# Kernel tuning notes

Hardware: AMD Instinct MI355X
Metric: run time of the kernel (lower is better)

Reference implementation:

```python
import jax, jax.numpy as jnp
import numpy as np

N, E = 30000, 180000
IN, H, OUT = 3000, 512, 30


def _segment_softmax(e, dst, n):
    # numerically stable softmax over incoming edges of each destination node
    m = jax.ops.segment_max(e, dst, num_segments=n)
    m = jnp.where(jnp.isfinite(m), m, 0.0)  # nodes with no in-edges
    ex = jnp.exp(e - m[dst])
    den = jax.ops.segment_sum(ex, dst, num_segments=n)
    return ex / den[dst]


def _gat(x, src, dst, Ws, Wd, a_s, a_d, n, alpha=None):
    """edGATConv (heads=1, no self-loops, no bias).
    xs = lin_s(x); attention score from lin_s(x)[src] and lin_d(x)[dst];
    out[i] = sum_{e: dst_e=i} alpha_e * xs[src_e].
    If alpha is given (tie_alpha), reuse it instead of recomputing."""
    xs = x @ Ws.T  # [n, F_out]
    if alpha is None:
        xd = x @ Wd.T
        e = jax.nn.leaky_relu(xs[src] @ a_s + xd[dst] @ a_d, 0.2)  # [E]
        alpha = _segment_softmax(e, dst, n)
    out = jax.ops.segment_sum(alpha[:, None] * xs[src], dst, num_segments=n)
    return out, alpha


def setup_inputs() -> dict:
    key = jax.random.key(0)
    ks = jax.random.split(key, 7)
    features = jax.random.normal(ks[0], (N, IN), dtype=jnp.float32)
    edge_index = jax.random.randint(ks[1], (2, E), 0, N)
    W1s = jax.random.normal(ks[2], (H, IN), dtype=jnp.float32) * 0.02
    W1d = jax.random.normal(ks[3], (H, IN), dtype=jnp.float32) * 0.02
    a1s = jax.random.normal(ks[4], (H,), dtype=jnp.float32) * 0.1
    a1d = jax.random.normal(ks[5], (H,), dtype=jnp.float32) * 0.1
    W2s = jax.random.normal(ks[6], (OUT, H), dtype=jnp.float32) * 0.05
    return {"features": features, "edge_index": edge_index,
            "W1s": W1s, "W1d": W1d, "a1s": a1s, "a1d": a1d, "W2s": W2s}


def reference(features, edge_index, W1s, W1d, a1s, a1d, W2s):
    src, dst = edge_index[0], edge_index[1]
    n = features.shape[0]
    # conv1: attentive GAT layer, stores tie_alpha
    h1, alpha1 = _gat(features, src, dst, W1s, W1d, a1s, a1d, n)
    h1 = jax.nn.elu(h1)
    # conv2: aslinear=True -> plain linear with lin_s
    h2 = h1 @ W2s.T  # [N, OUT]
    # conv3: weights tied to conv2 transposed, alpha tied to conv1
    # W3s = W2s.T so xs3 = h2 @ W3s.T = h2 @ W2s
    h3, _ = _gat(h2, src, dst, W2s.T, None, None, None, n, alpha=alpha1)
    h3 = jax.nn.elu(h3)
    # conv4: aslinear, weight tied to conv1 transposed: h3 @ W4s.T = h3 @ W1s
    h4 = h3 @ W1s  # [N, IN]
    return (h2, h4)
```

## Files before the change

kernel.cpp:

```cpp
#include <hip/hip_runtime.h>

typedef unsigned short u16;
typedef __bf16 bf16_t;
typedef bf16_t bf16x8 __attribute__((ext_vector_type(8)));
typedef float f32x4 __attribute__((ext_vector_type(4)));
typedef u16 u16x8 __attribute__((ext_vector_type(8)));

#define AS1 __attribute__((address_space(1)))
#define AS3 __attribute__((address_space(3)))

__device__ __forceinline__ u16 f2bf(float f) {
    union { float f; unsigned u; } v; v.f = f;
    unsigned r = v.u + 0x7FFFu + ((v.u >> 16) & 1u);
    return (u16)(r >> 16);
}
__device__ __forceinline__ float bf2f(u16 s) {
    union { unsigned u; float f; } v; v.u = ((unsigned)s) << 16;
    return v.f;
}

__device__ __forceinline__ void gload_lds16(const u16* g, u16* l) {
    __builtin_amdgcn_global_load_lds((AS1 const void*)g, (AS3 void*)l, 16, 0, 0);
}

template <bool OUT_BF16, bool GUARD>
__global__ __launch_bounds__(256) void gemm_bt(
    const u16* __restrict__ A, const u16* __restrict__ B, void* __restrict__ Cv,
    int K, int ldc, int Mreal, int Nreal)
{
    __shared__ u16 As[128 * 64];
    __shared__ u16 Bs[128 * 64];
    const int t = threadIdx.x;
    const int w = t >> 6, l = t & 63;

    const int nwg = gridDim.x * gridDim.y;
    const int lin = blockIdx.y * gridDim.x + blockIdx.x;
    const int xcd = lin & 7, loc = lin >> 3;
    const int q = nwg >> 3, r = nwg & 7;
    const int swz = (xcd < r ? xcd * (q + 1) : r * (q + 1) + (xcd - r) * q) + loc;
    const int bx = swz % gridDim.x, by = swz / gridDim.x;

    const int m0 = by * 128, n0 = bx * 128;
    const int wm = (w >> 1) * 64, wn = (w & 1) * 64;

    const int srow = w << 5;
    const int lrow = l >> 3, lc = l & 7;

    f32x4 acc[4][4] = {};

    for (int kt = 0; kt < K; kt += 64) {
#pragma unroll
        for (int i = 0; i < 4; ++i) {
            int row = srow + i * 8 + lrow;
            int gc = ((lc ^ (row & 7)) << 3);
            const u16* ga = A + (size_t)(m0 + row) * K + kt + gc;
            const u16* gb = B + (size_t)(n0 + row) * K + kt + gc;
            u16* la = &As[(srow + i * 8) * 64];
            u16* lb = &Bs[(srow + i * 8) * 64];
            gload_lds16(ga, la);
            gload_lds16(gb, lb);
        }
        asm volatile("s_waitcnt vmcnt(0)");
        __syncthreads();

#pragma unroll
        for (int kk = 0; kk < 2; ++kk) {
            bf16x8 af[4], bfr[4];
            int kc = kk * 4 + (l >> 4);
#pragma unroll
            for (int mi = 0; mi < 4; ++mi) {
                int row = wm + mi * 16 + (l & 15);
                af[mi] = *(const bf16x8*)&As[row * 64 + ((kc ^ (row & 7)) << 3)];
            }
#pragma unroll
            for (int ni = 0; ni < 4; ++ni) {
                int col = wn + ni * 16 + (l & 15);
                bfr[ni] = *(const bf16x8*)&Bs[col * 64 + ((kc ^ (col & 7)) << 3)];
            }
#pragma unroll
            for (int mi = 0; mi < 4; ++mi)
#pragma unroll
                for (int ni = 0; ni < 4; ++ni)
                    acc[mi][ni] = __builtin_amdgcn_mfma_f32_16x16x32_bf16(
                        af[mi], bfr[ni], acc[mi][ni], 0, 0, 0);
        }
        __syncthreads();
    }

#pragma unroll
    for (int mi = 0; mi < 4; ++mi) {
#pragma unroll
        for (int qq = 0; qq < 4; ++qq) {
            int row = m0 + wm + mi * 16 + (l >> 4) * 4 + qq;
            if (GUARD && row >= Mreal) continue;
#pragma unroll
            for (int ni = 0; ni < 4; ++ni) {
                int col = n0 + wn + ni * 16 + (l & 15);
                if (GUARD && col >= Nreal) continue;
                float v = acc[mi][ni][qq];
                if (OUT_BF16) ((u16*)Cv)[(size_t)row * ldc + col] = f2bf(v);
                else          ((float*)Cv)[(size_t)row * ldc + col] = v;
            }
        }
    }
}

__global__ void k_prep(const float* __restrict__ W1d, const float* __restrict__ a1d,
                       const float* __restrict__ W1s, const float* __restrict__ a1s,
                       const float* __restrict__ W2s, const int* __restrict__ dst,
                       float* __restrict__ vd, float* __restrict__ vs,
                       u16* __restrict__ w1sb, u16* __restrict__ w1st,
                       u16* __restrict__ w2sb, unsigned* __restrict__ deg) {
    int b = blockIdx.x, t = threadIdx.x;
    if (b < 12) {
        int i = b * 256 + t;
        if (i >= 3000) return;
        float ad = 0.f, as = 0.f;
        for (int h = 0; h < 512; ++h) {
            ad += W1d[(size_t)h * 3000 + i] * a1d[h];
            as += W1s[(size_t)h * 3000 + i] * a1s[h];
        }
        vd[i] = ad;
        vs[i] = as;
    } else if (b < 1516) {
        int idx = (b - 12) * 256 + t;
        int n = idx / 752, k = (idx % 752) * 4;
        ushort4 o = make_ushort4(0, 0, 0, 0);
        if (k < 3000) {
            float4 v = *(const float4*)(W1s + (size_t)n * 3000 + k);
            o.x = f2bf(v.x); o.y = f2bf(v.y); o.z = f2bf(v.z); o.w = f2bf(v.w);
        }
        *(ushort4*)(w1sb + (size_t)n * 3008 + k) = o;
    } else if (b < 1900) {
        __shared__ float tile[64][65];
        int fb = b - 1516;
        int i0 = (fb % 48) * 64, h0 = (fb / 48) * 64;
        int il = t & 63, hq = t >> 6;
#pragma unroll
        for (int rr = 0; rr < 16; ++rr) {
            int hl = rr * 4 + hq;
            int i = i0 + il;
            tile[hl][il] = (i < 3000) ? W1s[(size_t)(h0 + hl) * 3000 + i] : 0.f;
        }
        __syncthreads();
#pragma unroll
        for (int rr = 0; rr < 16; ++rr) {
            int il2 = rr * 4 + hq;
            w1st[(size_t)(i0 + il2) * 512 + h0 + il] = f2bf(tile[il][il2]);
        }
    } else if (b < 2156) {
        int idx = (b - 1900) * 256 + t;
        int n = idx >> 9, k = idx & 511;
        w2sb[idx] = (n < 30) ? f2bf(W2s[(size_t)n * 512 + k]) : (u16)0;
    } else {
        int j = (b - 2156) * 256 + t;
        if (j < 180000) atomicAdd(&deg[dst[j]], 1u);
    }
}

__global__ void k_convX(const float* __restrict__ X, u16* __restrict__ xb,
                        const float* __restrict__ vd, const float* __restrict__ vs,
                        float* __restrict__ sd, float* __restrict__ ss) {
    __shared__ float redd[4], reds[4];
    int n = blockIdx.x, t = threadIdx.x;
    u16* brow = xb + (size_t)n * 3008;
    if (n < 30000) {
        const float* xrow = X + (size_t)n * 3000;
        float pd = 0.f, ps = 0.f;
#pragma unroll
        for (int it = 0; it < 3; ++it) {
            int c = (t + it * 256) * 4;
            if (c < 3000) {
                float4 v = *(const float4*)(xrow + c);
                float4 wd = *(const float4*)(vd + c);
                float4 wvs = *(const float4*)(vs + c);
                ushort4 o;
                o.x = f2bf(v.x); o.y = f2bf(v.y); o.z = f2bf(v.z); o.w = f2bf(v.w);
                pd += v.x * wd.x + v.y * wd.y + v.z * wd.z + v.w * wd.w;
                ps += v.x * wvs.x + v.y * wvs.y + v.z * wvs.z + v.w * wvs.w;
                *(ushort4*)(brow + c) = o;
            } else if (c < 3008) {
                *(ushort4*)(brow + c) = make_ushort4(0, 0, 0, 0);
            }
        }
#pragma unroll
        for (int s = 32; s; s >>= 1) {
            pd += __shfl_xor(pd, s);
            ps += __shfl_xor(ps, s);
        }
        if ((t & 63) == 0) { redd[t >> 6] = pd; reds[t >> 6] = ps; }
        __syncthreads();
        if (t == 0) {
            sd[n] = redd[0] + redd[1] + redd[2] + redd[3];
            ss[n] = reds[0] + reds[1] + reds[2] + reds[3];
        }
    } else {
#pragma unroll
        for (int it = 0; it < 3; ++it) {
            int c = (t + it * 256) * 4;
            if (c < 3008) *(ushort4*)(brow + c) = make_ushort4(0, 0, 0, 0);
        }
    }
}

__global__ void k_scan1(const unsigned* __restrict__ deg, unsigned* __restrict__ bsum, int n) {
    __shared__ unsigned ws[4];
    int i = blockIdx.x * 256 + threadIdx.x;
    unsigned v = (i < n) ? deg[i] : 0u;
#pragma unroll
    for (int s = 32; s; s >>= 1) v += __shfl_xor(v, s);
    if ((threadIdx.x & 63) == 0) ws[threadIdx.x >> 6] = v;
    __syncthreads();
    if (threadIdx.x == 0) bsum[blockIdx.x] = ws[0] + ws[1] + ws[2] + ws[3];
}

__global__ void k_scanB(const unsigned* __restrict__ deg, const unsigned* __restrict__ bsum,
                        unsigned* __restrict__ off, unsigned* __restrict__ cur,
                        int n, int nb) {
    __shared__ unsigned tmp[256];
    __shared__ unsigned bo;
    int b = blockIdx.x, t = threadIdx.x, i = b * 256 + t;
    if (t < 64) {
        unsigned s0 = (t < nb) ? bsum[t] : 0u;
        unsigned s1 = (t + 64 < nb) ? bsum[t + 64] : 0u;
        unsigned v = ((t < b) ? s0 : 0u) + ((t + 64 < b) ? s1 : 0u);
#pragma unroll
        for (int s = 32; s; s >>= 1) v += __shfl_xor(v, s);
        if (t == 0) bo = v;
        if (b == nb - 1) {
            unsigned tv = s0 + s1;
#pragma unroll
            for (int s = 32; s; s >>= 1) tv += __shfl_xor(tv, s);
            if (t == 0) off[n] = tv;
        }
    }
    __syncthreads();
    unsigned v = (i < n) ? deg[i] : 0u;
    tmp[t] = v;
    __syncthreads();
    for (int s = 1; s < 256; s <<= 1) {
        unsigned a = (t >= s) ? tmp[t - s] : 0u;
        __syncthreads();
        tmp[t] += a;
        __syncthreads();
    }
    if (i < n) {
        unsigned o = bo + tmp[t] - v;
        off[i] = o;
        cur[i] = o;
    }
}

__global__ void k_fill(const int* __restrict__ dst, unsigned* __restrict__ cur,
                       unsigned* __restrict__ csr) {
    int j = blockIdx.x * 256 + threadIdx.x;
    if (j >= 180000) return;
    unsigned pos = atomicAdd(&cur[dst[j]], 1u);
    csr[pos] = (unsigned)j;
}

__global__ void k_soft(const int* __restrict__ src, const float* __restrict__ ss,
                       const float* __restrict__ sd, float* __restrict__ alpha,
                       const unsigned* __restrict__ csr, const unsigned* __restrict__ off) {
    int t = threadIdx.x;
    int g = t >> 3, l = t & 7;
    int n = blockIdx.x * 32 + g;
    if (n >= 30000) return;
    unsigned lo = off[n], hi = off[n + 1];
    if (lo == hi) return;
    float sdn = sd[n];
    float m = -1e30f;
    for (unsigned i = lo + l; i < hi; i += 8) {
        float v = ss[src[csr[i]]] + sdn;
        v = v > 0.f ? v : 0.2f * v;
        m = fmaxf(m, v);
    }
    m = fmaxf(m, __shfl_xor(m, 1));
    m = fmaxf(m, __shfl_xor(m, 2));
    m = fmaxf(m, __shfl_xor(m, 4));
    float den = 0.f;
    for (unsigned i = lo + l; i < hi; i += 8) {
        float v = ss[src[csr[i]]] + sdn;
        v = v > 0.f ? v : 0.2f * v;
        den += expf(v - m);
    }
    den += __shfl_xor(den, 1);
    den += __shfl_xor(den, 2);
    den += __shfl_xor(den, 4);
    float inv = 1.f / den;
    for (unsigned i = lo + l; i < hi; i += 8) {
        unsigned j = csr[i];
        float v = ss[src[j]] + sdn;
        v = v > 0.f ? v : 0.2f * v;
        alpha[j] = expf(v - m) * inv;
    }
}

__global__ void k_agg(const u16* __restrict__ xin, const float* __restrict__ alpha,
                      const unsigned* __restrict__ csr, const unsigned* __restrict__ off,
                      const int* __restrict__ src, u16* __restrict__ outb, int nvalid) {
    int w = threadIdx.x >> 6, l = threadIdx.x & 63;
    int n = blockIdx.x * 4 + w;
    float acc[8] = {};
    if (n < nvalid) {
        unsigned lo = off[n], hi = off[n + 1];
        unsigned i = lo;
        for (; i + 2 <= hi; i += 2) {
            unsigned j0 = csr[i], j1 = csr[i + 1];
            float a0 = alpha[j0], a1 = alpha[j1];
            int s0 = src[j0], s1 = src[j1];
            u16x8 r0 = *(const u16x8*)&xin[(size_t)s0 * 512 + l * 8];
            u16x8 r1 = *(const u16x8*)&xin[(size_t)s1 * 512 + l * 8];
#pragma unroll
            for (int k = 0; k < 8; ++k) acc[k] += a0 * bf2f(r0[k]) + a1 * bf2f(r1[k]);
        }
        if (i < hi) {
            unsigned j0 = csr[i];
            float a0 = alpha[j0];
            int s0 = src[j0];
            u16x8 r0 = *(const u16x8*)&xin[(size_t)s0 * 512 + l * 8];
#pragma unroll
            for (int k = 0; k < 8; ++k) acc[k] += a0 * bf2f(r0[k]);
        }
    }
    u16x8 o;
#pragma unroll
    for (int k = 0; k < 8; ++k) {
        float a = acc[k] > 0.f ? acc[k] : expf(acc[k]) - 1.f;
        o[k] = f2bf(a);
    }
    *(u16x8*)&outb[(size_t)n * 512 + l * 8] = o;
}

__global__ void k_xs3(const float* __restrict__ h2, const float* __restrict__ W2s,
                      u16* __restrict__ xs3) {
    int t = threadIdx.x;
    size_t n0 = (size_t)blockIdx.x * 8;
    float w0[30], w1[30];
#pragma unroll
    for (int o = 0; o < 30; ++o) {
        w0[o] = W2s[(size_t)o * 512 + t];
        w1[o] = W2s[(size_t)o * 512 + t + 256];
    }
    for (int r = 0; r < 8; ++r) {
        size_t n = n0 + r;
        const float* hr = h2 + n * 30;
        float a0 = 0.f, a1 = 0.f;
#pragma unroll
        for (int o = 0; o < 30; ++o) {
            float v = hr[o];
            a0 += v * w0[o];
            a1 += v * w1[o];
        }
        xs3[n * 512 + t] = f2bf(a0);
        xs3[n * 512 + t + 256] = f2bf(a1);
    }
}

extern "C" void kernel_launch(void* const* d_in, const int* in_sizes, int n_in,
                              void* d_out, int out_size, void* d_ws, size_t ws_size,
                              hipStream_t stream) {
    const float* X   = (const float*)d_in[0];
    const int*   ei  = (const int*)d_in[1];
    const float* W1s = (const float*)d_in[2];
    const float* W1d = (const float*)d_in[3];
    const float* a1s = (const float*)d_in[4];
    const float* a1d = (const float*)d_in[5];
    const float* W2s = (const float*)d_in[6];
    const int* src = ei;
    const int* dst = ei + 180000;

    float* out = (float*)d_out;
    float* h2 = out;
    float* h4 = out + 900000;

    char* ob = (char*)(out + 900000);
    u16* xbf  = (u16*)ob;
    u16* xs1b = (u16*)(ob + 180961280);
    u16* h1b  = (u16*)(ob + 180961280 + 30801920);
    u16* xs3b = (u16*)(ob + 180961280 + 30801920 + 30801920);

    char* w = (char*)d_ws;
    auto carve = [&](size_t bytes) { char* p = w; w += (bytes + 255) & ~(size_t)255; return p; };
    u16* w1sb  = (u16*)carve((size_t)512 * 3008 * 2);
    u16* w1st  = (u16*)carve((size_t)3072 * 512 * 2);
    u16* w2sb  = (u16*)carve((size_t)128 * 512 * 2);
    u16* h3b   = (u16*)carve((size_t)30080 * 512 * 2);
    float* vd    = (float*)carve(3008 * 4);
    float* vs    = (float*)carve(3008 * 4);
    float* ss    = (float*)carve(30000 * 4);
    float* sd    = (float*)carve(30000 * 4);
    float* alpha = (float*)carve(180000 * 4);
    unsigned* deg = (unsigned*)carve(30000 * 4);
    unsigned* off = (unsigned*)carve(30004 * 4);
    unsigned* cur = (unsigned*)carve(30000 * 4);
    unsigned* csr = (unsigned*)carve(180000 * 4);
    unsigned* bsum = (unsigned*)carve(128 * 4);

    hipMemsetAsync(deg, 0, 30000 * 4, stream);

    k_prep<<<2860, 256, 0, stream>>>(W1d, a1d, W1s, a1s, W2s, dst,
                                     vd, vs, w1sb, w1st, w2sb, deg);

    k_convX<<<30080, 256, 0, stream>>>(X, xbf, vd, vs, sd, ss);

    gemm_bt<true, false><<<dim3(4, 235), 256, 0, stream>>>(xbf, w1sb, xs1b, 3008, 512, 0, 0);

    k_scan1<<<118, 256, 0, stream>>>(deg, bsum, 30000);
    k_scanB<<<118, 256, 0, stream>>>(deg, bsum, off, cur, 30000, 118);
    k_fill<<<704, 256, 0, stream>>>(dst, cur, csr);
    k_soft<<<938, 256, 0, stream>>>(src, ss, sd, alpha, csr, off);

    k_agg <<<7520, 256, 0, stream>>>(xs1b, alpha, csr, off, src, h1b, 30000);

    gemm_bt<false, true><<<dim3(1, 235), 256, 0, stream>>>(h1b, w2sb, h2, 512, 30, 30000, 30);

    k_xs3 <<<3750, 256, 0, stream>>>(h2, W2s, xs3b);
    k_agg <<<7520, 256, 0, stream>>>(xs3b, alpha, csr, off, src, h3b, 30000);

    gemm_bt<false, true><<<dim3(24, 235), 256, 0, stream>>>(h3b, w1st, h4, 512, 3000, 30000, 3000);
}
```

Before: 681.5 us.

## Fuse X bf16 conversion into first GEMM and aggregate layer-3 before projection

The first GEMM now reads fp32 features directly, converts them to bf16 into LDS and computes the attention score dot products in the bx==0 blocks. This removes the separate conversion kernel and its write and re-read of a bf16 copy of X. Layer 3 is reordered to aggregate the 30-wide h2 over edges first and then project to 512 with ELU. This uses linearity to shrink the gather width from 512 bf16 to 30 fp32. The trade-off is redundant fp32 A-loads across the four column blocks, which read X four times.

Measured after the change: 645.5 us. -5.3%, faster.

```diff
diff --git a/kernel.cpp b/kernel.cpp
--- a/kernel.cpp
+++ b/kernel.cpp
@@ -103,6 +103,148 @@
             }
         }
     }
+}
+
+__global__ __launch_bounds__(256) void gemm_xw2(
+    const float* __restrict__ X, const u16* __restrict__ Bw, u16* __restrict__ C,
+    const float* __restrict__ vd, const float* __restrict__ vs,
+    float* __restrict__ sd, float* __restrict__ ss)
+{
+    __shared__ u16 As[128 * 64];
+    __shared__ u16 Bs[2][128 * 64];
+    const int t = threadIdx.x;
+    const int w = t >> 6, l = t & 63;
+
+    const int nwg = gridDim.x * gridDim.y;
+    const int lin = blockIdx.y * gridDim.x + blockIdx.x;
+    const int xcd = lin & 7, loc = lin >> 3;
+    const int q = nwg >> 3, r = nwg & 7;
+    const int swz = (xcd < r ? xcd * (q + 1) : r * (q + 1) + (xcd - r) * q) + loc;
+    const int bx = swz % gridDim.x, by = swz / gridDim.x;
+
+    const int m0 = by * 128, n0 = bx * 128;
+    const int wm = (w >> 1) * 64, wn = (w & 1) * 64;
+    const int srow = w << 5;
+    const int lrow = l >> 3, lc = l & 7;
+
+    f32x4 acc[4][4] = {};
+    float sdp[4] = {}, ssp[4] = {};
+    const bool do_s = (bx == 0);
+
+    int rowg[4];
+    bool okr[4];
+#pragma unroll
+    for (int i = 0; i < 4; ++i) {
+        rowg[i] = m0 + srow + i * 8 + lrow;
+        okr[i] = rowg[i] < 30000;
+    }
+
+    float4 pa[4][2];
+    auto loadA = [&](int kt) {
+        int c = kt + lc * 8;
+        bool okc = c < 3000;
+#pragma unroll
+        for (int i = 0; i < 4; ++i) {
+            bool ok = okr[i] && okc;
+            const float* p = X + (ok ? ((size_t)rowg[i] * 3000 + c) : 0);
+            float4 v0 = *(const float4*)p;
+            float4 v1 = *(const float4*)(p + 4);
+            if (!ok) { v0 = make_float4(0.f, 0.f, 0.f, 0.f); v1 = v0; }
+            pa[i][0] = v0;
+            pa[i][1] = v1;
+        }
+    };
+    auto stageB = [&](int kt2, int buf) {
+#pragma unroll
+        for (int i = 0; i < 4; ++i) {
+            int row = srow + i * 8 + lrow;
+            int gc = ((lc ^ (row & 7)) << 3);
+            gload_lds16(Bw + (size_t)(n0 + row) * 3008 + kt2 + gc,
+                        &Bs[buf][(srow + i * 8) * 64]);
+        }
+    };
+
+    loadA(0);
+    stageB(0, 0);
+    int cur = 0;
+
+    for (int kt = 0; kt < 3008; kt += 64) {
+        if (do_s) {
+            int c = kt + lc * 8;
+            float4 d0 = *(const float4*)(vd + c);
+            float4 d1 = *(const float4*)(vd + c + 4);
+            float4 s0 = *(const float4*)(vs + c);
+            float4 s1 = *(const float4*)(vs + c + 4);
+#pragma unroll
+            for (int i = 0; i < 4; ++i) {
+                sdp[i] += pa[i][0].x * d0.x + pa[i][0].y * d0.y + pa[i][0].z * d0.z + pa[i][0].w * d0.w
+                        + pa[i][1].x * d1.x + pa[i][1].y * d1.y + pa[i][1].z * d1.z + pa[i][1].w * d1.w;
+                ssp[i] += pa[i][0].x * s0.x + pa[i][0].y * s0.y + pa[i][0].z * s0.z + pa[i][0].w * s0.w
+                        + pa[i][1].x * s1.x + pa[i][1].y * s1.y + pa[i][1].z * s1.z + pa[i][1].w * s1.w;
+            }
+        }
+#pragma unroll
+        for (int i = 0; i < 4; ++i) {
+            int row = srow + i * 8 + lrow;
+            u16x8 o;
+            o[0] = f2bf(pa[i][0].x); o[1] = f2bf(pa[i][0].y);
+            o[2] = f2bf(pa[i][0].z); o[3] = f2bf(pa[i][0].w);
+            o[4] = f2bf(pa[i][1].x); o[5] = f2bf(pa[i][1].y);
+            o[6] = f2bf(pa[i][1].z); o[7] = f2bf(pa[i][1].w);
+            *(u16x8*)&As[row * 64 + ((lc ^ (row & 7)) << 3)] = o;
+        }
+        loadA(kt + 64);
+        int ktn = (kt + 64 < 3008) ? kt + 64 : 2944;
+        stageB(ktn, cur ^ 1);
+        asm volatile("s_waitcnt vmcnt(12) lgkmcnt(0)" ::: "memory");
+        __builtin_amdgcn_s_barrier();
+
+#pragma unroll
+        for (int kk = 0; kk < 2; ++kk) {
+            bf16x8 af[4], bfr[4];
+            int kc = kk * 4 + (l >> 4);
+#pragma unroll
+            for (int mi = 0; mi < 4; ++mi) {
+                int row = wm + mi * 16 + (l & 15);
+                af[mi] = *(const bf16x8*)&As[row * 64 + ((kc ^ (row & 7)) << 3)];
+            }
+#pragma unroll
+            for (int ni = 0; ni < 4; ++ni) {
+                int col = wn + ni * 16 + (l & 15);
+                bfr[ni] = *(const bf16x8*)&Bs[cur][col * 64 + ((kc ^ (col & 7)) << 3)];
+            }
+#pragma unroll
+            for (int mi = 0; mi < 4; ++mi)
+#pragma unroll
+                for (int ni = 0; ni < 4; ++ni)
+                    acc[mi][ni] = __builtin_amdgcn_mfma_f32_16x16x32_bf16(
+                        af[mi], bfr[ni], acc[mi][ni], 0, 0, 0);
+        }
+        asm volatile("s_barrier" ::: "memory");
+        cur ^= 1;
+    }
+
+    if (do_s) {
+#pragma unroll
+        for (int i = 0; i < 4; ++i) {
+            float a = sdp[i], b = ssp[i];
+            a += __shfl_xor(a, 1); a += __shfl_xor(a, 2); a += __shfl_xor(a, 4);
+            b += __shfl_xor(b, 1); b += __shfl_xor(b, 2); b += __shfl_xor(b, 4);
+            if (lc == 0 && okr[i]) { sd[rowg[i]] = a; ss[rowg[i]] = b; }
+        }
+    }
+
+#pragma unroll
+    for (int mi = 0; mi < 4; ++mi)
+#pragma unroll
+        for (int qq = 0; qq < 4; ++qq) {
+            int row = m0 + wm + mi * 16 + (l >> 4) * 4 + qq;
+#pragma unroll
+            for (int ni = 0; ni < 4; ++ni) {
+                int col = n0 + wn + ni * 16 + (l & 15);
+                C[(size_t)row * 512 + col] = f2bf(acc[mi][qq == 0 ? ni : ni][qq]);
+            }
+        }
 }
 
 __global__ void k_prep(const float* __restrict__ W1d, const float* __restrict__ a1d,
@@ -155,51 +297,6 @@
     } else {
         int j = (b - 2156) * 256 + t;
         if (j < 180000) atomicAdd(&deg[dst[j]], 1u);
-    }
-}
-
-__global__ void k_convX(const float* __restrict__ X, u16* __restrict__ xb,
-                        const float* __restrict__ vd, const float* __restrict__ vs,
-                        float* __restrict__ sd, float* __restrict__ ss) {
-    __shared__ float redd[4], reds[4];
-    int n = blockIdx.x, t = threadIdx.x;
-    u16* brow = xb + (size_t)n * 3008;
-    if (n < 30000) {
-        const float* xrow = X + (size_t)n * 3000;
-        float pd = 0.f, ps = 0.f;
-#pragma unroll
-        for (int it = 0; it < 3; ++it) {
-            int c = (t + it * 256) * 4;
-            if (c < 3000) {
-                float4 v = *(const float4*)(xrow + c);
-                float4 wd = *(const float4*)(vd + c);
-                float4 wvs = *(const float4*)(vs + c);
-                ushort4 o;
-                o.x = f2bf(v.x); o.y = f2bf(v.y); o.z = f2bf(v.z); o.w = f2bf(v.w);
-                pd += v.x * wd.x + v.y * wd.y + v.z * wd.z + v.w * wd.w;
-                ps += v.x * wvs.x + v.y * wvs.y + v.z * wvs.z + v.w * wvs.w;
-                *(ushort4*)(brow + c) = o;
-            } else if (c < 3008) {
-                *(ushort4*)(brow + c) = make_ushort4(0, 0, 0, 0);
-            }
-        }
-#pragma unroll
-        for (int s = 32; s; s >>= 1) {
-            pd += __shfl_xor(pd, s);
-            ps += __shfl_xor(ps, s);
-        }
-        if ((t & 63) == 0) { redd[t >> 6] = pd; reds[t >> 6] = ps; }
-        __syncthreads();
-        if (t == 0) {
-            sd[n] = redd[0] + redd[1] + redd[2] + redd[3];
-            ss[n] = reds[0] + reds[1] + reds[2] + reds[3];
-        }
-    } else {
-#pragma unroll
-        for (int it = 0; it < 3; ++it) {
-            int c = (t + it * 256) * 4;
-            if (c < 3008) *(ushort4*)(brow + c) = make_ushort4(0, 0, 0, 0);
-        }
     }
 }
 
@@ -332,8 +429,34 @@
     *(u16x8*)&outb[(size_t)n * 512 + l * 8] = o;
 }
 
-__global__ void k_xs3(const float* __restrict__ h2, const float* __restrict__ W2s,
-                      u16* __restrict__ xs3) {
+__global__ void k_aggG(const float* __restrict__ h2, const float* __restrict__ alpha,
+                       const unsigned* __restrict__ csr, const unsigned* __restrict__ off,
+                       const int* __restrict__ src, float* __restrict__ g) {
+    int t = threadIdx.x, grp = t >> 3, l = t & 7;
+    int n = blockIdx.x * 32 + grp;
+    if (n >= 30000) return;
+    unsigned lo = off[n], hi = off[n + 1];
+    float acc[4] = {};
+    int c0 = l * 4;
+    for (unsigned i = lo; i < hi; ++i) {
+        unsigned j = csr[i];
+        float a = alpha[j];
+        const float* row = h2 + (size_t)src[j] * 30;
+#pragma unroll
+        for (int k = 0; k < 4; ++k) {
+            int c = c0 + k;
+            if (c < 30) acc[k] += a * row[c];
+        }
+    }
+#pragma unroll
+    for (int k = 0; k < 4; ++k) {
+        int c = c0 + k;
+        if (c < 30) g[(size_t)n * 30 + c] = acc[k];
+    }
+}
+
+__global__ void k_h3(const float* __restrict__ g, const float* __restrict__ W2s,
+                     u16* __restrict__ h3b) {
     int t = threadIdx.x;
     size_t n0 = (size_t)blockIdx.x * 8;
     float w0[30], w1[30];
@@ -342,18 +465,22 @@
         w0[o] = W2s[(size_t)o * 512 + t];
         w1[o] = W2s[(size_t)o * 512 + t + 256];
     }
-    for (int r = 0; r < 8; ++r) {
-        size_t n = n0 + r;
-        const float* hr = h2 + n * 30;
+    for (int rr = 0; rr < 8; ++rr) {
+        size_t n = n0 + rr;
         float a0 = 0.f, a1 = 0.f;
-#pragma unroll
-        for (int o = 0; o < 30; ++o) {
-            float v = hr[o];
-            a0 += v * w0[o];
-            a1 += v * w1[o];
-        }
-        xs3[n * 512 + t] = f2bf(a0);
-        xs3[n * 512 + t + 256] = f2bf(a1);
+        if (n < 30000) {
+            const float* gr = g + n * 30;
+#pragma unroll
+            for (int o = 0; o < 30; ++o) {
+                float v = gr[o];
+                a0 += v * w0[o];
+                a1 += v * w1[o];
+            }
+            a0 = a0 > 0.f ? a0 : expf(a0) - 1.f;
+            a1 = a1 > 0.f ? a1 : expf(a1) - 1.f;
+        }
+        h3b[n * 512 + t] = f2bf(a0);
+        h3b[n * 512 + t + 256] = f2bf(a1);
     }
 }
 
@@ -375,10 +502,9 @@
     float* h4 = out + 900000;
 
     char* ob = (char*)(out + 900000);
-    u16* xbf  = (u16*)ob;
-    u16* xs1b = (u16*)(ob + 180961280);
-    u16* h1b  = (u16*)(ob + 180961280 + 30801920);
-    u16* xs3b = (u16*)(ob + 180961280 + 30801920 + 30801920);
+    u16* xs1b = (u16*)ob;
+    u16* h1b  = (u16*)(ob + 30801920);
+    float* g  = (float*)(ob + 30801920 + 30801920);
 
     char* w = (char*)d_ws;
     auto carve = [&](size_t bytes) { char* p = w; w += (bytes + 255) & ~(size_t)255; return p; };
@@ -402,9 +528,7 @@
     k_prep<<<2860, 256, 0, stream>>>(W1d, a1d, W1s, a1s, W2s, dst,
                                      vd, vs, w1sb, w1st, w2sb, deg);
 
-    k_convX<<<30080, 256, 0, stream>>>(X, xbf, vd, vs, sd, ss);
-
-    gemm_bt<true, false><<<dim3(4, 235), 256, 0, stream>>>(xbf, w1sb, xs1b, 3008, 512, 0, 0);
+    gemm_xw2<<<dim3(4, 235), 256, 0, stream>>>(X, w1sb, xs1b, vd, vs, sd, ss);
 
     k_scan1<<<118, 256, 0, stream>>>(deg, bsum, 30000);
     k_scanB<<<118, 256, 0, stream>>>(deg, bsum, off, cur, 30000, 118);
@@ -415,8 +539,8 @@
 
     gemm_bt<false, true><<<dim3(1, 235), 256, 0, stream>>>(h1b, w2sb, h2, 512, 30, 30000, 30);
 
-    k_xs3 <<<3750, 256, 0, stream>>>(h2, W2s, xs3b);
-    k_agg <<<7520, 256, 0, stream>>>(xs3b, alpha, csr, off, src, h3b, 30000);
+    k_aggG<<<938, 256, 0, stream>>>(h2, alpha, csr, off, src, g);
+    k_h3 <<<3760, 256, 0, stream>>>(g, W2s, h3b);
 
     gemm_bt<false, true><<<dim3(24, 235), 256, 0, stream>>>(h3b, w1st, h4, 512, 3000, 30000, 3000);
 }
```

## Aggregate 30-wide h2 before projecting to 512 in conv3

Applied to the files above, without the earlier changes.

Uses linearity to reorder conv3: the attention-weighted neighbour sum now runs over the 30-column h2 rows, and the W2s projection plus ELU are applied afterwards in a fused kernel that writes h3 directly. This replaces a 512-wide bf16 gather-aggregate over all edges with a 30-wide fp32 one, cutting gather traffic sharply. The xs3 intermediate buffer is dropped, and the projection now also zero-fills the padded rows up to 30080. Rounding changes because aggregation now happens in fp32 before the bf16 conversion.

After: 663.7 us. 2.6% less time.

```diff
diff --git a/kernel.cpp b/kernel.cpp
--- a/kernel.cpp
+++ b/kernel.cpp
@@ -332,8 +332,34 @@
     *(u16x8*)&outb[(size_t)n * 512 + l * 8] = o;
 }
 
-__global__ void k_xs3(const float* __restrict__ h2, const float* __restrict__ W2s,
-                      u16* __restrict__ xs3) {
+__global__ void k_aggG(const float* __restrict__ h2, const float* __restrict__ alpha,
+                       const unsigned* __restrict__ csr, const unsigned* __restrict__ off,
+                       const int* __restrict__ src, float* __restrict__ g) {
+    int t = threadIdx.x, grp = t >> 3, l = t & 7;
+    int n = blockIdx.x * 32 + grp;
+    if (n >= 30000) return;
+    unsigned lo = off[n], hi = off[n + 1];
+    float acc[4] = {};
+    int c0 = l * 4;
+    for (unsigned i = lo; i < hi; ++i) {
+        unsigned j = csr[i];
+        float a = alpha[j];
+        const float* row = h2 + (size_t)src[j] * 30;
+#pragma unroll
+        for (int k = 0; k < 4; ++k) {
+            int c = c0 + k;
+            if (c < 30) acc[k] += a * row[c];
+        }
+    }
+#pragma unroll
+    for (int k = 0; k < 4; ++k) {
+        int c = c0 + k;
+        if (c < 30) g[(size_t)n * 30 + c] = acc[k];
+    }
+}
+
+__global__ void k_h3(const float* __restrict__ g, const float* __restrict__ W2s,
+                     u16* __restrict__ h3b) {
     int t = threadIdx.x;
     size_t n0 = (size_t)blockIdx.x * 8;
     float w0[30], w1[30];
@@ -342,18 +368,22 @@
         w0[o] = W2s[(size_t)o * 512 + t];
         w1[o] = W2s[(size_t)o * 512 + t + 256];
     }
-    for (int r = 0; r < 8; ++r) {
-        size_t n = n0 + r;
-        const float* hr = h2 + n * 30;
+    for (int rr = 0; rr < 8; ++rr) {
+        size_t n = n0 + rr;
         float a0 = 0.f, a1 = 0.f;
-#pragma unroll
-        for (int o = 0; o < 30; ++o) {
-            float v = hr[o];
-            a0 += v * w0[o];
-            a1 += v * w1[o];
-        }
-        xs3[n * 512 + t] = f2bf(a0);
-        xs3[n * 512 + t + 256] = f2bf(a1);
+        if (n < 30000) {
+            const float* gr = g + n * 30;
+#pragma unroll
+            for (int o = 0; o < 30; ++o) {
+                float v = gr[o];
+                a0 += v * w0[o];
+                a1 += v * w1[o];
+            }
+            a0 = a0 > 0.f ? a0 : expf(a0) - 1.f;
+            a1 = a1 > 0.f ? a1 : expf(a1) - 1.f;
+        }
+        h3b[n * 512 + t] = f2bf(a0);
+        h3b[n * 512 + t + 256] = f2bf(a1);
     }
 }
 
@@ -378,7 +408,7 @@
     u16* xbf  = (u16*)ob;
     u16* xs1b = (u16*)(ob + 180961280);
     u16* h1b  = (u16*)(ob + 180961280 + 30801920);
-    u16* xs3b = (u16*)(ob + 180961280 + 30801920 + 30801920);
+    float* g  = (float*)(ob + 180961280 + 30801920 + 30801920);
 
     char* w = (char*)d_ws;
     auto carve = [&](size_t bytes) { char* p = w; w += (bytes + 255) & ~(size_t)255; return p; };
@@ -403,7 +433,6 @@
                                      vd, vs, w1sb, w1st, w2sb, deg);
 
     k_convX<<<30080, 256, 0, stream>>>(X, xbf, vd, vs, sd, ss);
-
     gemm_bt<true, false><<<dim3(4, 235), 256, 0, stream>>>(xbf, w1sb, xs1b, 3008, 512, 0, 0);
 
     k_scan1<<<118, 256, 0, stream>>>(deg, bsum, 30000);
@@ -415,8 +444,8 @@
 
     gemm_bt<false, true><<<dim3(1, 235), 256, 0, stream>>>(h1b, w2sb, h2, 512, 30, 30000, 30);
 
-    k_xs3 <<<3750, 256, 0, stream>>>(h2, W2s, xs3b);
-    k_agg <<<7520, 256, 0, stream>>>(xs3b, alpha, csr, off, src, h3b, 30000);
+    k_aggG<<<938, 256, 0, stream>>>(h2, alpha, csr, off, src, g);
+    k_h3 <<<3760, 256, 0, stream>>>(g, W2s, h3b);
 
     gemm_bt<false, true><<<dim3(24, 235), 256, 0, stream>>>(h3b, w1st, h4, 512, 3000, 30000, 3000);
 }
```
